# Kernel optimization log

Hardware: AMD Instinct MI355X
Metric: run time of the kernel (lower is better)

Reference implementation:

```python
import jax, jax.numpy as jnp
import numpy as np

N_NODES = 50000
N_EDGES = 800000
G_DIM = 128
H1 = 32
HEADS = 4
H2 = 64
ATT_SLOPE = 0.2   # PyG GATConv default negative_slope
LRELU_SLOPE = 0.01  # F.leaky_relu default
BN_EPS = 1e-5


def segment_softmax(logits, seg, num_segments):
    # numerically stable softmax over edges grouped by destination node
    m = jax.ops.segment_max(logits, seg, num_segments=num_segments)
    e = jnp.exp(logits - m[seg])
    s = jax.ops.segment_sum(e, seg, num_segments=num_segments)
    return e / (s[seg] + 1e-16)


def gat_layer(x, src, dst, W, a_src, a_dst, bias, concat):
    # PyG GATConv: x' = W x ; alpha_e = softmax_dst(leaky_relu(a_src.x_src + a_dst.x_dst))
    N = x.shape[0]
    H, C = a_src.shape
    xw = (x @ W).reshape(N, H, C)          # [N,H,C]
    al_s = jnp.sum(xw * a_src, axis=-1)    # [N,H]
    al_d = jnp.sum(xw * a_dst, axis=-1)    # [N,H]
    logits = jax.nn.leaky_relu(al_s[src] + al_d[dst], ATT_SLOPE)  # [E,H]
    alpha = segment_softmax(logits, dst, N)                        # [E,H]
    out = jax.ops.segment_sum(alpha[:, :, None] * xw[src], dst, num_segments=N)  # [N,H,C]
    out = out.reshape(N, H * C) if concat else out.mean(axis=1)
    return out + bias


def batchnorm_train(x, gamma, beta):
    mu = x.mean(axis=0)
    var = x.var(axis=0)  # biased, as torch BN uses for normalization
    return (x - mu) * jax.lax.rsqrt(var + BN_EPS) * gamma + beta


def setup_inputs() -> dict:
    key = jax.random.key(0)
    ks = jax.random.split(key, 12)
    node_features = jax.random.normal(ks[0], (N_NODES, G_DIM), dtype=jnp.float32)
    node_type = jax.random.randint(ks[1], (N_NODES,), 0, 3)
    edge_index = jax.random.randint(ks[2], (2, N_EDGES), 0, N_NODES)
    s1 = 1.0 / np.sqrt(G_DIM)
    s2 = 1.0 / np.sqrt(H1 * HEADS)
    return {
        "node_features": node_features,
        "node_type": node_type,
        "edge_index": edge_index,
        "W1": jax.random.normal(ks[3], (G_DIM, HEADS * H1), dtype=jnp.float32) * s1,
        "a_src1": jax.random.normal(ks[4], (HEADS, H1), dtype=jnp.float32) * s1,
        "a_dst1": jax.random.normal(ks[5], (HEADS, H1), dtype=jnp.float32) * s1,
        "b1": jnp.zeros((HEADS * H1,), dtype=jnp.float32),
        "g1": jnp.ones((HEADS * H1,), dtype=jnp.float32),
        "beta1": jnp.zeros((HEADS * H1,), dtype=jnp.float32),
        "W2": jax.random.normal(ks[6], (HEADS * H1, H2), dtype=jnp.float32) * s2,
        "a_src2": jax.random.normal(ks[7], (1, H2), dtype=jnp.float32) * s2,
        "a_dst2": jax.random.normal(ks[8], (1, H2), dtype=jnp.float32) * s2,
        "b2": jnp.zeros((H2,), dtype=jnp.float32),
        "g2": jnp.ones((H2,), dtype=jnp.float32),
        "beta2": jnp.zeros((H2,), dtype=jnp.float32),
    }


def reference(node_features, node_type, edge_index, W1, a_src1, a_dst1, b1, g1, beta1,
              W2, a_src2, a_dst2, b2, g2, beta2):
    N = node_features.shape[0]
    loop = jnp.arange(N)
    src = jnp.concatenate([edge_index[0], loop])  # add_self_loops=True (PyG default)
    dst = jnp.concatenate([edge_index[1], loop])
    x = gat_layer(node_features, src, dst, W1, a_src1, a_dst1, b1, concat=True)
    x = jax.nn.leaky_relu(batchnorm_train(x, g1, beta1), LRELU_SLOPE)
    x = gat_layer(x, src, dst, W2, a_src2, a_dst2, b2, concat=False)
    x = jax.nn.leaky_relu(batchnorm_train(x, g2, beta2), LRELU_SLOPE)
    return x
```

## Files before the change

kernel.cpp:

```cpp
#include <hip/hip_runtime.h>
#include <hip/hip_fp16.h>

#define NN 50000
#define NE 800000
#define ET 850000
#define GD 128
#define D1 128
#define NH 4
#define D2 64
#define NB_SCAN 196
#define NBP 1024
#define NXCD 8
#define NPX 6250
#define HB 3321

typedef unsigned short u16;
typedef _Float16 half8_t __attribute__((ext_vector_type(8)));
typedef float    f32x4_t __attribute__((ext_vector_type(4)));

__device__ __forceinline__ float lrelu(float x, float s) { return x > 0.f ? x : s * x; }

__global__ void k_prepw(const float* __restrict__ W1, const float* __restrict__ W2,
                        __half* __restrict__ Wp1, __half* __restrict__ Wp2,
                        int* __restrict__ cnt16) {
    int idx = blockIdx.x * 256 + threadIdx.x;
    if (idx < NN) cnt16[idx * 16] = 0;
    if (idx < 16384) {
        int i = idx & 7, l = (idx >> 3) & 63, nt = (idx >> 9) & 7, kk = idx >> 12;
        int k = kk * 32 + (l >> 4) * 8 + i, n = nt * 16 + (l & 15);
        Wp1[idx] = __float2half(W1[k * D1 + n]);
    } else if (idx < 24576) {
        int x2 = idx - 16384;
        int i = x2 & 7, l = (x2 >> 3) & 63, nt = (x2 >> 9) & 3, kk = x2 >> 11;
        int k = kk * 32 + (l >> 4) * 8 + i, n = nt * 16 + (l & 15);
        Wp2[x2] = __float2half(W2[k * D2 + n]);
    }
}

__global__ void k_histgemm1(const int* __restrict__ ei, int* __restrict__ cnt16,
                            u16* __restrict__ pos16,
                            const float* __restrict__ x, const half8_t* __restrict__ wp,
                            const float* __restrict__ as, const float* __restrict__ ad,
                            __half* __restrict__ xw, float* __restrict__ al_s,
                            float* __restrict__ al_d) {
    if (blockIdx.x < HB) {
        int e = blockIdx.x * 256 + threadIdx.x;
        if (e < ET) {
            int d = (e < NE) ? ei[NE + e] : (e - NE);
            int pos = atomicAdd(&cnt16[d * 16], 1);
            pos16[e] = (u16)pos;
        }
        return;
    }
    const int strip = (blockIdx.x - HB) * 4 + (threadIdx.x >> 6);
    if (strip >= NN / 16) return;
    const int l = threadIdx.x & 63;
    const int row0 = strip * 16;
    const int c = l & 15, g = l >> 4;
    const float* xrow = x + (size_t)(row0 + c) * GD;

    f32x4_t acc[8];
#pragma unroll
    for (int nt = 0; nt < 8; nt++) acc[nt] = (f32x4_t){0.f, 0.f, 0.f, 0.f};

#pragma unroll
    for (int kk = 0; kk < 4; kk++) {
        const int koff = kk * 32 + g * 8;
        f32x4_t a0 = *(const f32x4_t*)(xrow + koff);
        f32x4_t a1 = *(const f32x4_t*)(xrow + koff + 4);
        half8_t af;
#pragma unroll
        for (int i = 0; i < 4; i++) { af[i] = (_Float16)a0[i]; af[i + 4] = (_Float16)a1[i]; }
#pragma unroll
        for (int nt = 0; nt < 8; nt++) {
            half8_t bf = wp[(kk * 8 + nt) * 64 + l];
            acc[nt] = __builtin_amdgcn_mfma_f32_16x16x32_f16(af, bf, acc[nt], 0, 0, 0);
        }
    }

    float asv[8], adv[8];
#pragma unroll
    for (int nt = 0; nt < 8; nt++) { asv[nt] = as[nt * 16 + c]; adv[nt] = ad[nt * 16 + c]; }

#pragma unroll
    for (int r = 0; r < 4; r++) {
        const int row = row0 + g * 4 + r;
        __half* xwr = xw + (size_t)row * D1;
        float hs[4] = {0.f, 0.f, 0.f, 0.f}, hd[4] = {0.f, 0.f, 0.f, 0.f};
#pragma unroll
        for (int nt = 0; nt < 8; nt++) {
            float v = acc[nt][r];
            xwr[nt * 16 + c] = __float2half(v);
            hs[nt >> 1] += v * asv[nt];
            hd[nt >> 1] += v * adv[nt];
        }
#pragma unroll
        for (int m = 1; m <= 8; m <<= 1) {
#pragma unroll
            for (int h = 0; h < 4; h++) { hs[h] += __shfl_xor(hs[h], m); hd[h] += __shfl_xor(hd[h], m); }
        }
        if (c == 0) {
#pragma unroll
            for (int h = 0; h < 4; h++) { al_s[row * NH + h] = hs[h]; al_d[row * NH + h] = hd[h]; }
        }
    }
}

__global__ void k_blocksum(const int* __restrict__ cnt16, int* __restrict__ part) {
    __shared__ int r[256];
    int t = threadIdx.x, i = blockIdx.x * 256 + t;
    r[t] = (i < NN) ? cnt16[i * 16] : 0;
    __syncthreads();
    for (int s = 128; s >= 1; s >>= 1) {
        if (t < s) r[t] += r[t + s];
        __syncthreads();
    }
    if (t == 0) part[blockIdx.x] = r[0];
}

__global__ void k_scanfix(const int* __restrict__ cnt16, const int* __restrict__ part,
                          int* __restrict__ row_ptr) {
    __shared__ int pp[256];
    __shared__ int r[256];
    int b = blockIdx.x, t = threadIdx.x, i = b * 256 + t;
    pp[t] = (t < NB_SCAN) ? part[t] : 0;
    int v = (i < NN) ? cnt16[i * 16] : 0;
    r[t] = v;
    __syncthreads();
    for (int off = 1; off < 256; off <<= 1) {
        int pv = (t >= off) ? pp[t - off] : 0;
        int rv = (t >= off) ? r[t - off] : 0;
        __syncthreads();
        pp[t] += pv; r[t] += rv;
        __syncthreads();
    }
    int pbase = b ? pp[b - 1] : 0;
    if (i < NN) row_ptr[i] = pbase + (t ? r[t - 1] : 0);
    if (i == NN - 1) row_ptr[NN] = pbase + r[t];
}

__global__ void k_fill_x(const int* __restrict__ ei, const int* __restrict__ row_ptr,
                         const u16* __restrict__ pos16, u16* __restrict__ csr_src) {
    const int xcd = blockIdx.x & (NXCD - 1);
    const int grp = blockIdx.x >> 3;
    const int ngrp = gridDim.x >> 3;
    const int lo = xcd * NPX, hi = lo + NPX;
    for (int e = grp * 256 + threadIdx.x; e < ET; e += ngrp * 256) {
        int d = (e < NE) ? ei[NE + e] : (e - NE);
        if (d >= lo && d < hi) {
            int s = (e < NE) ? ei[e] : d;
            csr_src[row_ptr[d] + pos16[e]] = (u16)s;
        }
    }
}

__global__ void k_gat1(const int* __restrict__ row_ptr, const u16* __restrict__ csr_src,
                       const float* __restrict__ als, const float* __restrict__ ald,
                       const __half2* __restrict__ xw, __half2* __restrict__ out) {
    const int b = blockIdx.x;
    const int d = (b & (NXCD - 1)) * NPX + (b >> 3);
    const int beg = row_ptr[d];
    const int deg = row_ptr[d + 1] - beg;
    const int lane = threadIdx.x;

    __shared__ int   s_src[64];
    __shared__ float s_al[64 * NH];

    const float4 adv = *(const float4*)(ald + d * NH);
    const int h = lane >> 4;

    float ax = 0.f, ay = 0.f, den = 0.f;
    for (int base = 0; base < deg; base += 64) {
        int cnt = min(64, deg - base);
        if (lane < cnt) {
            int s = csr_src[beg + base + lane];
            s_src[lane] = s;
            const float4 a = *(const float4*)(als + s * NH);
            s_al[lane * NH + 0] = __expf(lrelu(a.x + adv.x, 0.2f));
            s_al[lane * NH + 1] = __expf(lrelu(a.y + adv.y, 0.2f));
            s_al[lane * NH + 2] = __expf(lrelu(a.z + adv.z, 0.2f));
            s_al[lane * NH + 3] = __expf(lrelu(a.w + adv.w, 0.2f));
        }
        __syncthreads();
#pragma unroll 4
        for (int i = 0; i < cnt; i++) {
            float al = s_al[i * NH + h];
            float2 v = __half22float2(xw[(size_t)s_src[i] * 64 + lane]);
            den += al; ax += al * v.x; ay += al * v.y;
        }
        __syncthreads();
    }
    float inv = 1.f / (den + 1e-16f);
    __half2 hv;
    hv.x = __float2half(ax * inv);
    hv.y = __float2half(ay * inv);
    out[(size_t)d * 64 + lane] = hv;
}

__global__ void k_bnstats1h(const __half2* __restrict__ x, float* __restrict__ bp) {
    int t = threadIdx.x, bid = blockIdx.x;
    float s0 = 0.f, q0 = 0.f, s1 = 0.f, q1 = 0.f;
    for (int r = bid; r < NN; r += NBP) {
        float2 f = __half22float2(x[(size_t)r * 64 + t]);
        s0 += f.x; q0 += f.x * f.x;
        s1 += f.y; q1 += f.y * f.y;
    }
    bp[bid * D1 + 2 * t] = s0;
    bp[bid * D1 + 2 * t + 1] = s1;
    bp[NBP * D1 + bid * D1 + 2 * t] = q0;
    bp[NBP * D1 + bid * D1 + 2 * t + 1] = q1;
}

template <int D>
__global__ void k_bnstats(const float* __restrict__ x, float* __restrict__ bp) {
    int j = threadIdx.x, bid = blockIdx.x;
    float s = 0.f, q = 0.f;
    for (int r = bid; r < NN; r += NBP) {
        float v = x[(size_t)r * D + j];
        s += v; q += v * v;
    }
    bp[bid * D + j] = s;
    bp[NBP * D + bid * D + j] = q;
}

template <int D>
__global__ void k_bnreduce(const float* __restrict__ bp, const float* __restrict__ g,
                           const float* __restrict__ b, float* __restrict__ scale,
                           float* __restrict__ shift) {
    __shared__ float rs[256], rq[256];
    int j = blockIdx.x, t = threadIdx.x;
    float s = 0.f, q = 0.f;
    for (int i = t; i < NBP; i += 256) {
        s += bp[i * D + j];
        q += bp[NBP * D + i * D + j];
    }
    rs[t] = s; rq[t] = q;
    __syncthreads();
    for (int st = 128; st >= 1; st >>= 1) {
        if (t < st) { rs[t] += rs[t + st]; rq[t] += rq[t + st]; }
        __syncthreads();
    }
    if (t == 0) {
        float mu = rs[0] / (float)NN;
        float var = rq[0] / (float)NN - mu * mu;
        float sc = rsqrtf(var + 1e-5f) * g[j];
        scale[j] = sc;
        shift[j] = b[j] - mu * sc;
    }
}

__global__ void k_bnapply2(const float* __restrict__ x, const float* __restrict__ scale,
                           const float* __restrict__ shift, float* __restrict__ y) {
    int idx = blockIdx.x * blockDim.x + threadIdx.x;
    if (idx >= NN * D2 / 4) return;
    float4 v = ((const float4*)x)[idx];
    int c = (idx * 4) & (D2 - 1);
    v.x = lrelu(v.x * scale[c + 0] + shift[c + 0], 0.01f);
    v.y = lrelu(v.y * scale[c + 1] + shift[c + 1], 0.01f);
    v.z = lrelu(v.z * scale[c + 2] + shift[c + 2], 0.01f);
    v.w = lrelu(v.w * scale[c + 3] + shift[c + 3], 0.01f);
    ((float4*)y)[idx] = v;
}

__global__ void k_gemm2m(const __half* __restrict__ x, const float* __restrict__ scale,
                         const float* __restrict__ shift, const half8_t* __restrict__ wp,
                         const float* __restrict__ as, const float* __restrict__ ad,
                         __half* __restrict__ xw, float* __restrict__ al_s, float* __restrict__ al_d) {
    const int l = threadIdx.x;
    const int row0 = blockIdx.x * 16;
    const int c = l & 15, g = l >> 4;
    const __half* xrow = x + (size_t)(row0 + c) * D1;

    f32x4_t acc[4];
#pragma unroll
    for (int nt = 0; nt < 4; nt++) acc[nt] = (f32x4_t){0.f, 0.f, 0.f, 0.f};

#pragma unroll
    for (int kk = 0; kk < 4; kk++) {
        const int koff = kk * 32 + g * 8;
        half8_t a8 = *(const half8_t*)(xrow + koff);
        f32x4_t sc0 = *(const f32x4_t*)(scale + koff);
        f32x4_t sc1 = *(const f32x4_t*)(scale + koff + 4);
        f32x4_t sh0 = *(const f32x4_t*)(shift + koff);
        f32x4_t sh1 = *(const f32x4_t*)(shift + koff + 4);
        half8_t af;
#pragma unroll
        for (int i = 0; i < 4; i++) {
            af[i]     = (_Float16)lrelu((float)a8[i] * sc0[i] + sh0[i], 0.01f);
            af[i + 4] = (_Float16)lrelu((float)a8[i + 4] * sc1[i] + sh1[i], 0.01f);
        }
#pragma unroll
        for (int nt = 0; nt < 4; nt++) {
            half8_t bf = wp[(kk * 4 + nt) * 64 + l];
            acc[nt] = __builtin_amdgcn_mfma_f32_16x16x32_f16(af, bf, acc[nt], 0, 0, 0);
        }
    }

    float asv[4], adv[4];
#pragma unroll
    for (int nt = 0; nt < 4; nt++) { asv[nt] = as[nt * 16 + c]; adv[nt] = ad[nt * 16 + c]; }

#pragma unroll
    for (int r = 0; r < 4; r++) {
        const int row = row0 + g * 4 + r;
        __half* xwr = xw + (size_t)row * D2;
        float hs = 0.f, hd = 0.f;
#pragma unroll
        for (int nt = 0; nt < 4; nt++) {
            float v = acc[nt][r];
            xwr[nt * 16 + c] = __float2half(v);
            hs += v * asv[nt];
            hd += v * adv[nt];
        }
#pragma unroll
        for (int m = 1; m <= 8; m <<= 1) { hs += __shfl_xor(hs, m); hd += __shfl_xor(hd, m); }
        if (c == 0) { al_s[row] = hs; al_d[row] = hd; }
    }
}

__global__ void k_gat2(const int* __restrict__ row_ptr, const u16* __restrict__ csr_src,
                       const float* __restrict__ als, const float* __restrict__ ald,
                       const __half2* __restrict__ xw, float* __restrict__ out) {
    const int b = blockIdx.x;
    const int d = (b & (NXCD - 1)) * NPX + (b >> 3);
    const int beg = row_ptr[d];
    const int deg = row_ptr[d + 1] - beg;
    const int lane = threadIdx.x;
    const int sub = lane >> 5, l = lane & 31;

    const float add = ald[d];
    float ax = 0.f, ay = 0.f, den = 0.f;
    for (int base = 0; base < deg; base += 64) {
        int cnt = min(64, deg - base);
        int s = 0; float e = 0.f;
        if (lane < cnt) {
            s = csr_src[beg + base + lane];
            e = __expf(lrelu(als[s] + add, 0.2f));
        }
        int np = (cnt + 1) >> 1;
        for (int i = 0; i < np; i++) {
            int idx = 2 * i + sub;
            float al = __shfl(e, idx);
            int  si  = __shfl(s, idx);
            float2 v = __half22float2(xw[(size_t)si * 32 + l]);
            den += al; ax += al * v.x; ay += al * v.y;
        }
    }
    ax += __shfl_xor(ax, 32); ay += __shfl_xor(ay, 32); den += __shfl_xor(den, 32);
    if (lane < 32) {
        float inv = 1.f / (den + 1e-16f);
        *(float2*)(out + (size_t)d * D2 + 2 * l) = make_float2(ax * inv, ay * inv);
    }
}

extern "C" void kernel_launch(void* const* d_in, const int* in_sizes, int n_in,
                              void* d_out, int out_size, void* d_ws, size_t ws_size,
                              hipStream_t stream) {
    const float* x   = (const float*)d_in[0];
    const int*   ei  = (const int*)d_in[2];
    const float* W1  = (const float*)d_in[3];
    const float* as1 = (const float*)d_in[4];
    const float* ad1 = (const float*)d_in[5];
    const float* g1  = (const float*)d_in[7];
    const float* be1 = (const float*)d_in[8];
    const float* W2  = (const float*)d_in[9];
    const float* as2 = (const float*)d_in[10];
    const float* ad2 = (const float*)d_in[11];
    const float* g2  = (const float*)d_in[13];
    const float* be2 = (const float*)d_in[14];
    float* out = (float*)d_out;

    float* ws = (float*)d_ws;
    __half* xw1  = (__half*)ws;
    __half* xw2  = (__half*)ws;
    float* bp    = ws + 1600000;
    float* al_s2 = ws + 3200000;
    float* al_d2 = ws + 3250000;
    float* al_s1 = ws + 6400000;
    float* al_d1 = al_s1 + 200000;
    float* aggF  = al_d1 + 200000;
    __half* agg1 = (__half*)aggF;
    u16*   pos16 = (u16*)aggF;
    int*   cnt16 = (int*)(aggF + 425008);
    float* aggE  = aggF + 6400000 / 2 * 2;
    int*   row_ptr = (int*)(al_d1 + 200000 + 6400000);
    int*   part    = row_ptr + 50001;
    float* st      = (float*)(part + 249);
    u16*   csr_src = (u16*)(st + 768);
    __half* Wp1    = (__half*)(csr_src + 850000);
    __half* Wp2    = Wp1 + 16384;
    (void)aggE;

    k_prepw<<<196, 256, 0, stream>>>(W1, W2, Wp1, Wp2, cnt16);
    k_histgemm1<<<HB + (NN / 16 + 3) / 4, 256, 0, stream>>>(ei, cnt16, pos16, x,
                                                            (const half8_t*)Wp1,
                                                            as1, ad1, xw1, al_s1, al_d1);
    k_blocksum<<<NB_SCAN, 256, 0, stream>>>(cnt16, part);
    k_scanfix<<<NB_SCAN, 256, 0, stream>>>(cnt16, part, row_ptr);
    k_fill_x<<<4096, 256, 0, stream>>>(ei, row_ptr, pos16, csr_src);

    k_gat1<<<NN, 64, 0, stream>>>(row_ptr, csr_src, al_s1, al_d1, (const __half2*)xw1,
                                  (__half2*)agg1);
    k_bnstats1h<<<NBP, 64, 0, stream>>>((const __half2*)agg1, bp);
    k_bnreduce<D1><<<D1, 256, 0, stream>>>(bp, g1, be1, st, st + 128);

    k_gemm2m<<<NN / 16, 64, 0, stream>>>(agg1, st, st + 128, (const half8_t*)Wp2, as2, ad2,
                                         xw2, al_s2, al_d2);
    k_gat2<<<NN, 64, 0, stream>>>(row_ptr, csr_src, al_s2, al_d2, (const __half2*)xw2, out);
    k_bnstats<D2><<<NBP, D2, 0, stream>>>(out, bp);
    k_bnreduce<D2><<<D2, 256, 0, stream>>>(bp, g2, be2, st + 256, st + 320);
    k_bnapply2<<<(NN * D2 / 4 + 255) / 256, 256, 0, stream>>>(out, st + 256, st + 320, out);
}
```

Baseline: 197.6 us.

## Build CSR with per-block LDS histograms and compacted edge lists instead of global atomics

Replaces the global-atomic per-destination histogram and the full edge rescan in fill with 256 blocks. Each block handles one node slice and one edge slice, keeps a shared-memory histogram of local positions, and appends its matching edges compactly to a per-block list. A new per-node prefix pass over the 32 edge slices gives each node's slice offsets, and fill then scatters only the compacted entries. This is meant to cut contended global atomics and repeated edge reads, at the cost of an extra kernel, extra workspace, and a fixed per-block capacity (CAP 8192) that random inputs are assumed not to exceed.

```diff
diff --git a/kernel.cpp b/kernel.cpp
--- a/kernel.cpp
+++ b/kernel.cpp
@@ -12,7 +12,10 @@
 #define NBP 1024
 #define NXCD 8
 #define NPX 6250
-#define HB 3321
+#define NSB 32
+#define ESL 26563
+#define NHB 256
+#define CAP 8192
 
 typedef unsigned short u16;
 typedef _Float16 half8_t __attribute__((ext_vector_type(8)));
@@ -21,10 +24,8 @@
 __device__ __forceinline__ float lrelu(float x, float s) { return x > 0.f ? x : s * x; }
 
 __global__ void k_prepw(const float* __restrict__ W1, const float* __restrict__ W2,
-                        __half* __restrict__ Wp1, __half* __restrict__ Wp2,
-                        int* __restrict__ cnt16) {
+                        __half* __restrict__ Wp1, __half* __restrict__ Wp2) {
     int idx = blockIdx.x * 256 + threadIdx.x;
-    if (idx < NN) cnt16[idx * 16] = 0;
     if (idx < 16384) {
         int i = idx & 7, l = (idx >> 3) & 63, nt = (idx >> 9) & 7, kk = idx >> 12;
         int k = kk * 32 + (l >> 4) * 8 + i, n = nt * 16 + (l & 15);
@@ -37,22 +38,41 @@
     }
 }
 
-__global__ void k_histgemm1(const int* __restrict__ ei, int* __restrict__ cnt16,
-                            u16* __restrict__ pos16,
+__global__ void k_histgemm1(const int* __restrict__ ei,
+                            unsigned* __restrict__ ulist, u16* __restrict__ plist,
+                            int* __restrict__ partial, int* __restrict__ mcount,
                             const float* __restrict__ x, const half8_t* __restrict__ wp,
                             const float* __restrict__ as, const float* __restrict__ ad,
                             __half* __restrict__ xw, float* __restrict__ al_s,
                             float* __restrict__ al_d) {
-    if (blockIdx.x < HB) {
-        int e = blockIdx.x * 256 + threadIdx.x;
-        if (e < ET) {
+    __shared__ unsigned lh[NPX];
+    __shared__ unsigned lk;
+    if (blockIdx.x < NHB) {
+        const int s = blockIdx.x & (NXCD - 1), j = blockIdx.x >> 3;
+        const int lo = s * NPX;
+        for (int i = threadIdx.x; i < NPX; i += 256) lh[i] = 0u;
+        if (threadIdx.x == 0) lk = 0u;
+        __syncthreads();
+        const int e0 = j * ESL, e1 = min(ET, e0 + ESL);
+        const size_t ub = (size_t)blockIdx.x * CAP;
+        for (int e = e0 + threadIdx.x; e < e1; e += 256) {
             int d = (e < NE) ? ei[NE + e] : (e - NE);
-            int pos = atomicAdd(&cnt16[d * 16], 1);
-            pos16[e] = (u16)pos;
-        }
+            unsigned dl = (unsigned)(d - lo);
+            if (dl < (unsigned)NPX) {
+                unsigned p = atomicAdd(&lh[dl], 1u);
+                int src = (e < NE) ? ei[e] : d;
+                unsigned k = atomicAdd(&lk, 1u);
+                ulist[ub + k] = (dl << 16) | (unsigned)src;
+                plist[ub + k] = (u16)p;
+            }
+        }
+        __syncthreads();
+        const size_t pb = ((size_t)s * NSB + j) * NPX;
+        for (int i = threadIdx.x; i < NPX; i += 256) partial[pb + i] = (int)lh[i];
+        if (threadIdx.x == 0) mcount[blockIdx.x] = (int)lk;
         return;
     }
-    const int strip = (blockIdx.x - HB) * 4 + (threadIdx.x >> 6);
+    const int strip = (blockIdx.x - NHB) * 4 + (threadIdx.x >> 6);
     if (strip >= NN / 16) return;
     const int l = threadIdx.x & 63;
     const int row0 = strip * 16;
@@ -106,10 +126,25 @@
     }
 }
 
-__global__ void k_blocksum(const int* __restrict__ cnt16, int* __restrict__ part) {
+__global__ void k_nodeprefix(const int* __restrict__ partial, int* __restrict__ P,
+                             int* __restrict__ cnt) {
+    int d = blockIdx.x * 256 + threadIdx.x;
+    if (d >= NN) return;
+    int s = d / NPX, dl = d - s * NPX;
+    size_t base = (size_t)s * NSB * NPX + dl;
+    int run = 0;
+    for (int j = 0; j < NSB; j++) {
+        size_t idx = base + (size_t)j * NPX;
+        P[idx] = run;
+        run += partial[idx];
+    }
+    cnt[d] = run;
+}
+
+__global__ void k_blocksum(const int* __restrict__ cnt, int* __restrict__ part) {
     __shared__ int r[256];
     int t = threadIdx.x, i = blockIdx.x * 256 + t;
-    r[t] = (i < NN) ? cnt16[i * 16] : 0;
+    r[t] = (i < NN) ? cnt[i] : 0;
     __syncthreads();
     for (int s = 128; s >= 1; s >>= 1) {
         if (t < s) r[t] += r[t + s];
@@ -118,13 +153,13 @@
     if (t == 0) part[blockIdx.x] = r[0];
 }
 
-__global__ void k_scanfix(const int* __restrict__ cnt16, const int* __restrict__ part,
+__global__ void k_scanfix(const int* __restrict__ cnt, const int* __restrict__ part,
                           int* __restrict__ row_ptr) {
     __shared__ int pp[256];
     __shared__ int r[256];
     int b = blockIdx.x, t = threadIdx.x, i = b * 256 + t;
     pp[t] = (t < NB_SCAN) ? part[t] : 0;
-    int v = (i < NN) ? cnt16[i * 16] : 0;
+    int v = (i < NN) ? cnt[i] : 0;
     r[t] = v;
     __syncthreads();
     for (int off = 1; off < 256; off <<= 1) {
@@ -139,18 +174,21 @@
     if (i == NN - 1) row_ptr[NN] = pbase + r[t];
 }
 
-__global__ void k_fill_x(const int* __restrict__ ei, const int* __restrict__ row_ptr,
-                         const u16* __restrict__ pos16, u16* __restrict__ csr_src) {
-    const int xcd = blockIdx.x & (NXCD - 1);
-    const int grp = blockIdx.x >> 3;
-    const int ngrp = gridDim.x >> 3;
-    const int lo = xcd * NPX, hi = lo + NPX;
-    for (int e = grp * 256 + threadIdx.x; e < ET; e += ngrp * 256) {
-        int d = (e < NE) ? ei[NE + e] : (e - NE);
-        if (d >= lo && d < hi) {
-            int s = (e < NE) ? ei[e] : d;
-            csr_src[row_ptr[d] + pos16[e]] = (u16)s;
-        }
+__global__ void k_fill_x(const int* __restrict__ row_ptr, const int* __restrict__ P,
+                         const unsigned* __restrict__ ulist, const u16* __restrict__ plist,
+                         const int* __restrict__ mcount, u16* __restrict__ csr_src) {
+    const int b = blockIdx.x;
+    const int s = b & (NXCD - 1), j = b >> 3;
+    const int lo = s * NPX;
+    const int m = mcount[b];
+    const size_t ub = (size_t)b * CAP;
+    const size_t pb = ((size_t)s * NSB + j) * NPX;
+    for (int k = threadIdx.x; k < m; k += 256) {
+        unsigned u = ulist[ub + k];
+        unsigned p = plist[ub + k];
+        int dl = (int)(u >> 16);
+        int base = row_ptr[lo + dl] + P[pb + dl];
+        csr_src[base + p] = (u16)(u & 0xffffu);
     }
 }
 
@@ -374,30 +412,32 @@
     __half* xw1  = (__half*)ws;
     __half* xw2  = (__half*)ws;
     float* bp    = ws + 1600000;
+    unsigned* ulist = (unsigned*)(ws + 3200000);
+    u16*   plist  = (u16*)(ws + 5297152);
+    int*   mcount = (int*)(ws + 6345728);
+    int*   cnt    = (int*)(ws + 6345984);
     float* al_s2 = ws + 3200000;
     float* al_d2 = ws + 3250000;
     float* al_s1 = ws + 6400000;
     float* al_d1 = al_s1 + 200000;
     float* aggF  = al_d1 + 200000;
     __half* agg1 = (__half*)aggF;
-    u16*   pos16 = (u16*)aggF;
-    int*   cnt16 = (int*)(aggF + 425008);
-    float* aggE  = aggF + 6400000 / 2 * 2;
-    int*   row_ptr = (int*)(al_d1 + 200000 + 6400000);
+    int*   partial = (int*)aggF;
+    int*   Pbase   = (int*)(aggF + 1600000);
+    int*   row_ptr = (int*)(aggF + 3200000);
     int*   part    = row_ptr + 50001;
     float* st      = (float*)(part + 249);
     u16*   csr_src = (u16*)(st + 768);
     __half* Wp1    = (__half*)(csr_src + 850000);
     __half* Wp2    = Wp1 + 16384;
-    (void)aggE;
-
-    k_prepw<<<196, 256, 0, stream>>>(W1, W2, Wp1, Wp2, cnt16);
-    k_histgemm1<<<HB + (NN / 16 + 3) / 4, 256, 0, stream>>>(ei, cnt16, pos16, x,
-                                                            (const half8_t*)Wp1,
-                                                            as1, ad1, xw1, al_s1, al_d1);
-    k_blocksum<<<NB_SCAN, 256, 0, stream>>>(cnt16, part);
-    k_scanfix<<<NB_SCAN, 256, 0, stream>>>(cnt16, part, row_ptr);
-    k_fill_x<<<4096, 256, 0, stream>>>(ei, row_ptr, pos16, csr_src);
+
+    k_prepw<<<96, 256, 0, stream>>>(W1, W2, Wp1, Wp2);
+    k_histgemm1<<<NHB + (NN / 16 + 3) / 4, 256, 0, stream>>>(
+        ei, ulist, plist, partial, mcount, x, (const half8_t*)Wp1, as1, ad1, xw1, al_s1, al_d1);
+    k_nodeprefix<<<NB_SCAN, 256, 0, stream>>>(partial, Pbase, cnt);
+    k_blocksum<<<NB_SCAN, 256, 0, stream>>>(cnt, part);
+    k_scanfix<<<NB_SCAN, 256, 0, stream>>>(cnt, part, row_ptr);
+    k_fill_x<<<NHB, 256, 0, stream>>>(row_ptr, Pbase, ulist, plist, mcount, csr_src);
 
     k_gat1<<<NN, 64, 0, stream>>>(row_ptr, csr_src, al_s1, al_d1, (const __half2*)xw1,
                                   (__half2*)agg1);
```

Result: slower. 213.5 us (+8.1%).
